# Kernel optimization log

Hardware: AMD Instinct MI355X
Metric: run time of the kernel (lower is better)

The kernel has to match this reference:

```python
import jax, jax.numpy as jnp
import numpy as np
import math

H, E, HD = 12, 768, 64   # heads, embed_dim, per-head hidden
B, S, L = 8, 512, 512    # batch, dec len, enc len
EPS = 1e-12


def layer_norm(x, w, b):
    u = jnp.mean(x, axis=-1, keepdims=True)
    s = jnp.mean((x - u) ** 2, axis=-1, keepdims=True)
    return w * (x - u) / jnp.sqrt(s + EPS) + b


def gelu(x):
    return x * 0.5 * (1.0 + jax.lax.erf(x / math.sqrt(2.0)))


def attention(k, q, w_k, w_q, pw, pb, mask):
    # k:[b,kl,E] q:[b,ql,E] w_k/w_q:[H,E,HD] mask broadcastable to [b,H,ql,kl]
    kx = jnp.einsum('ble,hed->bhld', k, w_k)
    qx = jnp.einsum('bqe,hed->bhqd', q, w_q)
    score = jnp.einsum('bhqd,bhkd->bhqk', qx, kx) / math.sqrt(HD)
    score = jnp.where(mask, score, jnp.asarray(-1e4, score.dtype))
    attn = jax.nn.softmax(score, axis=-1)
    out = jnp.einsum('bhqk,bhkd->bhqd', attn, kx)  # values are kx (as in source)
    b_, h, ql, d = out.shape
    out = out.transpose(0, 2, 1, 3).reshape(b_, ql, h * d)
    return out @ pw + pb


def setup_inputs() -> dict:
    key = jax.random.key(0)
    ks = jax.random.split(key, 16)
    xav = lambda k, shp, fan: jax.random.normal(k, shp, jnp.float32) * math.sqrt(2.0 / fan)
    inp = {
        'X': jax.random.normal(ks[0], (B, S, E), jnp.float32),
        'enc_outputs': jax.random.normal(ks[1], (B, L, E), jnp.float32),
        'enc_valid_lens': jax.random.randint(ks[2], (B,), 1, L + 1, jnp.int32),
        'w_kx1': xav(ks[3], (H, E, HD), E + HD),
        'w_qx1': xav(ks[4], (H, E, HD), E + HD),
        'proj1_w': xav(ks[5], (H * HD, E), 2 * E),
        'proj1_b': jnp.zeros((E,), jnp.float32),
        'ln1_w': jnp.ones((E,), jnp.float32),
        'ln1_b': jnp.zeros((E,), jnp.float32),
        'w_kx2': xav(ks[6], (H, E, HD), E + HD),
        'w_qx2': xav(ks[7], (H, E, HD), E + HD),
        'proj2_w': xav(ks[8], (H * HD, E), 2 * E),
        'proj2_b': jnp.zeros((E,), jnp.float32),
        'ln2_w': jnp.ones((E,), jnp.float32),
        'ln2_b': jnp.zeros((E,), jnp.float32),
        'ffn_w1': xav(ks[9], (E, E), 2 * E),
        'ffn_b1': jnp.zeros((E,), jnp.float32),
        'ffn_w2': xav(ks[10], (E, E), 2 * E),
        'ffn_b2': jnp.zeros((E,), jnp.float32),
        'ln3_w': jnp.ones((E,), jnp.float32),
        'ln3_b': jnp.zeros((E,), jnp.float32),
    }
    return inp


def reference(X, enc_outputs, enc_valid_lens,
              w_kx1, w_qx1, proj1_w, proj1_b, ln1_w, ln1_b,
              w_kx2, w_qx2, proj2_w, proj2_b, ln2_w, ln2_b,
              ffn_w1, ffn_b1, ffn_w2, ffn_b2, ln3_w, ln3_b):
    s = X.shape[1]
    # training path: dec_valid_lens is 2D -> causal mask in Attention
    causal = jnp.tril(jnp.ones((s, s), dtype=bool))[None, None]          # [1,1,s,s]
    X2 = attention(X, X, w_kx1, w_qx1, proj1_w, proj1_b, causal)
    Y = layer_norm(X2 + X, ln1_w, ln1_b)
    # cross mask: key padding from enc_valid_lens (1D branch)
    kl = enc_outputs.shape[1]
    pad = (jnp.arange(kl)[None] < enc_valid_lens[:, None])[:, None, None]  # [b,1,1,kl]
    Y2 = attention(enc_outputs, Y, w_kx2, w_qx2, proj2_w, proj2_b, pad)
    Z = layer_norm(Y2 + Y, ln2_w, ln2_b)
    F = gelu(Z @ ffn_w1 + ffn_b1) @ ffn_w2 + ffn_b2
    return layer_norm(F + Z, ln3_w, ln3_b)
```

## Files before the change

kernel.cpp:

```cpp
#include <hip/hip_runtime.h>
#include <hip/hip_bf16.h>

typedef __hip_bfloat16 bf16;
typedef __attribute__((ext_vector_type(8))) short s8v;
typedef __attribute__((ext_vector_type(4))) short s4v;
typedef __attribute__((ext_vector_type(4))) float f4v;

#define H_ 12
#define E_ 768
#define HD_ 64
#define B_ 8
#define S_ 512
#define M_ 4096

struct P9 { const void* s[8]; bf16* d[8]; const void* vs[10]; bf16* vd[10]; };

typedef __attribute__((address_space(3))) void lds_void;
typedef const __attribute__((address_space(1))) void g_void;

__device__ __forceinline__ void async_copy16(const bf16* g, short* l) {
    __builtin_amdgcn_global_load_lds((g_void*)g, (lds_void*)l, 16, 0, 0);
}

__device__ __forceinline__ float sh2f(short v) {
    unsigned int u = ((unsigned int)(unsigned short)v) << 16;
    return __uint_as_float(u);
}

__global__ void detect_kernel(const unsigned int* __restrict__ X, int* flag) {
    __shared__ int cnt;
    if (threadIdx.x == 0) cnt = 0;
    __syncthreads();
    int good = 0;
    for (int i = threadIdx.x; i < 16384; i += 256) {
        unsigned e = (X[i] >> 7) & 0xFFu;
        good += (e >= 100u && e <= 141u) ? 1 : 0;
    }
    atomicAdd(&cnt, good);
    __syncthreads();
    if (threadIdx.x == 0) *flag = (cnt > 9830) ? 0 : 1;
}

__global__ void conv2_kernel(const void* s0, const void* s1, bf16* d0, bf16* d1,
                             const int* __restrict__ flag) {
    const int fp32 = *flag;
    const void* s = blockIdx.y ? s1 : s0;
    bf16* d = blockIdx.y ? d1 : d0;
    int i = (blockIdx.x * 256 + threadIdx.x) * 4;
    if (fp32) {
        float4 v = *(const float4*)((const float*)s + i);
        bf16 a = __float2bfloat16(v.x), b = __float2bfloat16(v.y),
             c = __float2bfloat16(v.z), e = __float2bfloat16(v.w);
        s4v o = { *(short*)&a, *(short*)&b, *(short*)&c, *(short*)&e };
        *(s4v*)(d + i) = o;
    } else {
        *(s4v*)(d + i) = *(const s4v*)((const bf16*)s + i);
    }
}

__device__ __forceinline__ bf16 ldcvt(const void* s, int i, int fp32) {
    return fp32 ? __float2bfloat16(((const float*)s)[i]) : ((const bf16*)s)[i];
}

__global__ void repack_kernel(P9 p, const int* __restrict__ flag) {
    const int fp32 = *flag;
    const int z = blockIdx.z;
    if (z == 8) {
        int id = blockIdx.y * 12 + blockIdx.x;
        if (id < 10) {
            const void* s = p.vs[id];
            bf16* d = p.vd[id];
            for (int i = threadIdx.x; i < E_; i += 256) d[i] = ldcvt(s, i, fp32);
        }
        return;
    }
    __shared__ float t[64][65];
    const int c = threadIdx.x & 63, r0 = threadIdx.x >> 6;
    if (z < 4) {
        const void* s = p.s[z];
        bf16* d = p.d[z];
        const int e0 = blockIdx.x * 64, h = blockIdx.y;
        #pragma unroll
        for (int j = 0; j < 16; ++j) {
            int r = r0 * 16 + j;
            int idx = (h * E_ + e0 + r) * HD_ + c;
            t[r][c] = fp32 ? ((const float*)s)[idx] : __bfloat162float(((const bf16*)s)[idx]);
        }
        __syncthreads();
        #pragma unroll
        for (int j = 0; j < 16; ++j) {
            int r = r0 * 16 + j;
            d[(size_t)(h * 64 + r) * E_ + e0 + c] = __float2bfloat16(t[c][r]);
        }
    } else {
        const void* s = p.s[z];
        bf16* d = p.d[z];
        const int k0 = blockIdx.x * 64, n0 = blockIdx.y * 64;
        #pragma unroll
        for (int j = 0; j < 16; ++j) {
            int r = r0 * 16 + j;
            int idx = (k0 + r) * E_ + n0 + c;
            t[r][c] = fp32 ? ((const float*)s)[idx] : __bfloat162float(((const bf16*)s)[idx]);
        }
        __syncthreads();
        #pragma unroll
        for (int j = 0; j < 16; ++j) {
            int r = r0 * 16 + j;
            d[(size_t)(n0 + r) * E_ + k0 + c] = __float2bfloat16(t[c][r]);
        }
    }
}

__global__ void ktrans_kernel(const bf16* __restrict__ K1, const bf16* __restrict__ K2,
                              bf16* __restrict__ KT1, bf16* __restrict__ KT2) {
    __shared__ short t[64 * 72];
    const bf16* src = blockIdx.z ? K2 : K1;
    bf16* dst = blockIdx.z ? KT2 : KT1;
    const int s0 = blockIdx.x * 64, bh = blockIdx.y;
    const int b = bh / H_, h = bh % H_;
    const int tid = threadIdx.x;
    #pragma unroll
    for (int it = 0; it < 2; ++it) {
        int idx = tid * 2 + it;
        int row = idx >> 3, ch = (idx & 7) * 8;
        s8v v = *(const s8v*)(src + ((size_t)(b * S_ + s0 + row) * H_ + h) * HD_ + ch);
        *(s8v*)&t[row * 72 + ch] = v;
    }
    __syncthreads();
    const int orow = tid >> 2, oc = (tid & 3) * 16;
    s8v o0, o1;
    #pragma unroll
    for (int j = 0; j < 8; ++j) o0[j] = t[(oc + j) * 72 + orow];
    #pragma unroll
    for (int j = 0; j < 8; ++j) o1[j] = t[(oc + 8 + j) * 72 + orow];
    bf16* dp = dst + (size_t)(bh * 64 + orow) * S_ + s0 + oc;
    *(s8v*)dp = o0;
    *(s8v*)(dp + 8) = o1;
}

template <int EPI>
__global__ __launch_bounds__(256, 4) void gemm4(const bf16* __restrict__ A,
                                                const bf16* __restrict__ Aalt,
                                                const bf16* __restrict__ Bt,
                                                bf16* __restrict__ C,
                                                bf16* __restrict__ C2,
                                                bf16* __restrict__ C3,
                                                const bf16* __restrict__ bias,
                                                const bf16* __restrict__ res) {
    __shared__ short As[64 * 64];
    __shared__ short Bs[96 * 64];
    const int bm = blockIdx.x, bn = blockIdx.y;
    const int tid = threadIdx.x;
    const int w = tid >> 6, l = tid & 63;
    const int wr = (w >> 1) * 32, wc = (w & 1) * 48;
    const int lc = l & 15, quad = l >> 4;
    const int srA = l >> 3, slot = l & 7;
    const int kc = (slot ^ srA) * 8;

    const bf16* Ap = (EPI == 3 && bn >= 16) ? Aalt : A;

    f4v acc[2][3] = {};

    for (int k0 = 0; k0 < E_; k0 += 64) {
        #pragma unroll
        for (int c = 0; c < 5; ++c) {
            int seg = w * 5 + c;
            if (seg < 8) {
                int row = seg * 8 + srA;
                async_copy16(Ap + (size_t)(bm * 64 + row) * E_ + k0 + kc, &As[seg * 512]);
            } else {
                int row = (seg - 8) * 8 + srA;
                async_copy16(Bt + (size_t)(bn * 96 + row) * E_ + k0 + kc, &Bs[(seg - 8) * 512]);
            }
        }
        __syncthreads();

        #pragma unroll
        for (int kk = 0; kk < 2; ++kk) {
            s8v a[2], b[3];
            #pragma unroll
            for (int t = 0; t < 2; ++t) {
                int ar = wr + t * 16 + lc;
                a[t] = *(const s8v*)&As[ar * 64 + (((kk * 4 + quad) ^ (ar & 7)) * 8)];
            }
            #pragma unroll
            for (int t = 0; t < 3; ++t) {
                int bc = wc + t * 16 + lc;
                b[t] = *(const s8v*)&Bs[bc * 64 + (((kk * 4 + quad) ^ (bc & 7)) * 8)];
            }
            #pragma unroll
            for (int mt = 0; mt < 2; ++mt)
                #pragma unroll
                for (int nt = 0; nt < 3; ++nt)
                    acc[mt][nt] = __builtin_amdgcn_mfma_f32_16x16x32_bf16(a[mt], b[nt], acc[mt][nt], 0, 0, 0);
        }
        __syncthreads();
    }

    bf16* Co = C;
    int coff = 0;
    if (EPI == 3) {
        if (bn < 8)       { Co = C;  coff = 0; }
        else if (bn < 16) { Co = C2; coff = 768; }
        else              { Co = C3; coff = 1536; }
    }

    #pragma unroll
    for (int mt = 0; mt < 2; ++mt)
        #pragma unroll
        for (int nt = 0; nt < 3; ++nt)
            #pragma unroll
            for (int i = 0; i < 4; ++i) {
                int row = bm * 64 + wr + mt * 16 + quad * 4 + i;
                int col = bn * 96 + wc + nt * 16 + lc;
                float v = acc[mt][nt][i];
                if (EPI == 1)
                    v += __bfloat162float(bias[col]) + __bfloat162float(res[(size_t)row * E_ + col]);
                if (EPI == 2) {
                    v += __bfloat162float(bias[col]);
                    v = 0.5f * v * (1.0f + erff(v * 0.70710678118654752f));
                }
                if (EPI == 3) Co[(size_t)row * E_ + (col - coff)] = __float2bfloat16(v);
                else          C[(size_t)row * E_ + col] = __float2bfloat16(v);
            }
}

template <bool CAUSAL>
__global__ __launch_bounds__(256) void attn_kernel(const bf16* __restrict__ Q,
                                                   const bf16* __restrict__ Kx,
                                                   const bf16* __restrict__ KT,
                                                   bf16* __restrict__ O,
                                                   const int* __restrict__ vlen) {
    __shared__ short qs[64 * 64];
    __shared__ short ks[64 * 64];
    __shared__ short kts[64 * 64];
    __shared__ short ps[64 * 72];

    const int bh = blockIdx.x, qt = blockIdx.y;
    const int h = bh % H_, b = bh / H_;
    const int tid = threadIdx.x, w = tid >> 6, l = tid & 63;
    const int lr = (l >> 4) * 4, lc = l & 15, quad = l >> 4;
    const int srA = l >> 3, slot = l & 7;
    const int kc = (slot ^ srA) * 8;

    #pragma unroll
    for (int c = 0; c < 2; ++c) {
        int seg = w * 2 + c;
        int row = seg * 8 + srA;
        async_copy16(Q + ((size_t)(b * S_ + qt * 64 + row) * H_ + h) * HD_ + kc, &qs[seg * 512]);
    }

    const int valid = CAUSAL ? S_ : vlen[b];
    const int kmax = CAUSAL ? (qt + 1) : ((valid + 63) >> 6);

    float m_i[4], l_i[4];
    for (int i = 0; i < 4; i++) { m_i[i] = -3.0e38f; l_i[i] = 0.0f; }
    f4v o_acc[4] = {};

    for (int kt = 0; kt < kmax; ++kt) {
        #pragma unroll
        for (int c = 0; c < 2; ++c) {
            int seg = w * 2 + c;
            int row = seg * 8 + srA;
            async_copy16(Kx + ((size_t)(b * S_ + kt * 64 + row) * H_ + h) * HD_ + kc, &ks[seg * 512]);
            async_copy16(KT + (size_t)(bh * 64 + row) * S_ + kt * 64 + kc, &kts[seg * 512]);
        }
        __syncthreads();

        f4v sacc[4] = {};
        const int rq = w * 16 + lc;
        s8v aq0 = *(const s8v*)&qs[rq * 64 + ((quad ^ (rq & 7)) * 8)];
        s8v aq1 = *(const s8v*)&qs[rq * 64 + (((4 + quad) ^ (rq & 7)) * 8)];
        #pragma unroll
        for (int nt = 0; nt < 4; nt++) {
            int rk = nt * 16 + lc;
            s8v bk0 = *(const s8v*)&ks[rk * 64 + ((quad ^ (rk & 7)) * 8)];
            s8v bk1 = *(const s8v*)&ks[rk * 64 + (((4 + quad) ^ (rk & 7)) * 8)];
            sacc[nt] = __builtin_amdgcn_mfma_f32_16x16x32_bf16(aq0, bk0, sacc[nt], 0, 0, 0);
            sacc[nt] = __builtin_amdgcn_mfma_f32_16x16x32_bf16(aq1, bk1, sacc[nt], 0, 0, 0);
        }

        #pragma unroll
        for (int i = 0; i < 4; i++) {
            int qabs = qt * 64 + w * 16 + lr + i;
            float sv[4];
            float mx = -3.0e38f;
            #pragma unroll
            for (int nt = 0; nt < 4; nt++) {
                int kabs = kt * 64 + nt * 16 + lc;
                float s = sacc[nt][i] * 0.125f;
                bool ok = CAUSAL ? (kabs <= qabs) : (kabs < valid);
                sv[nt] = ok ? s : -1.0e4f;
                mx = fmaxf(mx, sv[nt]);
            }
            #pragma unroll
            for (int off = 1; off < 16; off <<= 1) mx = fmaxf(mx, __shfl_xor(mx, off));
            float mnew = fmaxf(m_i[i], mx);
            float alpha = __expf(m_i[i] - mnew);
            float psum = 0.0f;
            #pragma unroll
            for (int nt = 0; nt < 4; nt++) {
                float p = __expf(sv[nt] - mnew);
                psum += p;
                *(bf16*)&ps[(w * 16 + lr + i) * 72 + nt * 16 + lc] = __float2bfloat16(p);
            }
            #pragma unroll
            for (int off = 1; off < 16; off <<= 1) psum += __shfl_xor(psum, off);
            l_i[i] = l_i[i] * alpha + psum;
            m_i[i] = mnew;
            #pragma unroll
            for (int dt = 0; dt < 4; dt++) o_acc[dt][i] *= alpha;
        }

        s8v ap0 = *(const s8v*)&ps[rq * 72 + quad * 8];
        s8v ap1 = *(const s8v*)&ps[rq * 72 + 32 + quad * 8];
        #pragma unroll
        for (int dt = 0; dt < 4; dt++) {
            int rd = dt * 16 + lc;
            s8v bv0 = *(const s8v*)&kts[rd * 64 + ((quad ^ (rd & 7)) * 8)];
            s8v bv1 = *(const s8v*)&kts[rd * 64 + (((4 + quad) ^ (rd & 7)) * 8)];
            o_acc[dt] = __builtin_amdgcn_mfma_f32_16x16x32_bf16(ap0, bv0, o_acc[dt], 0, 0, 0);
            o_acc[dt] = __builtin_amdgcn_mfma_f32_16x16x32_bf16(ap1, bv1, o_acc[dt], 0, 0, 0);
        }
        __syncthreads();
    }

    #pragma unroll
    for (int dt = 0; dt < 4; dt++)
        #pragma unroll
        for (int i = 0; i < 4; i++) {
            int q = qt * 64 + w * 16 + lr + i;
            int d = dt * 16 + lc;
            float v = o_acc[dt][i] / l_i[i];
            O[((size_t)(b * S_ + q) * H_ + h) * HD_ + d] = __float2bfloat16(v);
        }
}

__global__ __launch_bounds__(256) void ln2_kernel(const bf16* __restrict__ X,
                                                  const bf16* __restrict__ wv,
                                                  const bf16* __restrict__ bv,
                                                  bf16* __restrict__ outb,
                                                  float* __restrict__ outf,
                                                  const int* __restrict__ flag) {
    const int row = blockIdx.x * 4 + (threadIdx.x >> 6);
    const int l = threadIdx.x & 63;
    const bf16* xr = X + (size_t)row * E_;
    s8v v8 = *(const s8v*)(xr + l * 8);
    s4v v4 = *(const s4v*)(xr + 512 + l * 4);
    float x[12];
    #pragma unroll
    for (int j = 0; j < 8; ++j) x[j] = sh2f(v8[j]);
    #pragma unroll
    for (int j = 0; j < 4; ++j) x[8 + j] = sh2f(v4[j]);
    float s = 0.f, ss = 0.f;
    #pragma unroll
    for (int j = 0; j < 12; ++j) { s += x[j]; ss += x[j] * x[j]; }
    #pragma unroll
    for (int off = 1; off < 64; off <<= 1) {
        s += __shfl_xor(s, off);
        ss += __shfl_xor(ss, off);
    }
    float mu = s * (1.0f / E_);
    float var = ss * (1.0f / E_) - mu * mu;
    float rstd = rsqrtf(fmaxf(var, 0.0f) + 1e-12f);
    const bool f32out = (outf != nullptr) && (*flag != 0);
    #pragma unroll
    for (int j = 0; j < 12; ++j) {
        int c = (j < 8) ? (l * 8 + j) : (512 + l * 4 + (j - 8));
        float v = (x[j] - mu) * rstd * __bfloat162float(wv[c]) + __bfloat162float(bv[c]);
        if (f32out) outf[(size_t)row * E_ + c] = v;
        else        outb[(size_t)row * E_ + c] = __float2bfloat16(v);
    }
}

extern "C" void kernel_launch(void* const* d_in, const int* in_sizes, int n_in,
                              void* d_out, int out_size, void* d_ws, size_t ws_size,
                              hipStream_t stream) {
    const void* X = d_in[0];
    const void* enc = d_in[1];
    const int* vlen = (const int*)d_in[2];

    char* ws = (char*)d_ws;
    int* flag = (int*)ws;
    bf16* vecs = (bf16*)(ws + 256);
    char* wbase = ws + 16384;
    const size_t WSZ = (size_t)E_ * E_ * sizeof(bf16);
    bf16* wk1 = (bf16*)(wbase + 0 * WSZ);
    bf16* wq1 = (bf16*)(wbase + 1 * WSZ);
    bf16* wk2 = (bf16*)(wbase + 2 * WSZ);
    bf16* wq2 = (bf16*)(wbase + 3 * WSZ);
    bf16* p1t = (bf16*)(wbase + 4 * WSZ);
    bf16* p2t = (bf16*)(wbase + 5 * WSZ);
    bf16* f1t = (bf16*)(wbase + 6 * WSZ);
    bf16* f2t = (bf16*)(wbase + 7 * WSZ);
    const size_t ASZ = (size_t)M_ * E_ * sizeof(bf16);
    char* abase = wbase + 8 * WSZ;
    bf16* Xc   = (bf16*)(abase + 0 * ASZ);
    bf16* ENCc = (bf16*)(abase + 1 * ASZ);
    bf16* A0  = (bf16*)(abase + 2 * ASZ);
    bf16* A1  = (bf16*)(abase + 3 * ASZ);
    bf16* A2  = (bf16*)(abase + 4 * ASZ);
    bf16* A3  = (bf16*)(abase + 5 * ASZ);
    bf16* A4  = (bf16*)(abase + 6 * ASZ);
    bf16* A5  = (bf16*)(abase + 7 * ASZ);
    bf16* KT1 = (bf16*)(abase + 8 * ASZ);
    bf16* KT2 = (bf16*)(abase + 9 * ASZ);

    bf16* bias1 = vecs + 0 * E_;
    bf16* lw1   = vecs + 1 * E_;
    bf16* lb1   = vecs + 2 * E_;
    bf16* bias2 = vecs + 3 * E_;
    bf16* lw2   = vecs + 4 * E_;
    bf16* lb2   = vecs + 5 * E_;
    bf16* fb1   = vecs + 6 * E_;
    bf16* fb2   = vecs + 7 * E_;
    bf16* lw3   = vecs + 8 * E_;
    bf16* lb3   = vecs + 9 * E_;

    detect_kernel<<<1, 256, 0, stream>>>((const unsigned int*)X, flag);
    conv2_kernel<<<dim3(M_ * E_ / 1024, 2), 256, 0, stream>>>(X, enc, Xc, ENCc, flag);

    P9 rp;
    rp.s[0] = d_in[3];  rp.d[0] = wk1;
    rp.s[1] = d_in[4];  rp.d[1] = wq1;
    rp.s[2] = d_in[9];  rp.d[2] = wk2;
    rp.s[3] = d_in[10]; rp.d[3] = wq2;
    rp.s[4] = d_in[5];  rp.d[4] = p1t;
    rp.s[5] = d_in[11]; rp.d[5] = p2t;
    rp.s[6] = d_in[15]; rp.d[6] = f1t;
    rp.s[7] = d_in[17]; rp.d[7] = f2t;
    rp.vs[0] = d_in[6];  rp.vd[0] = bias1;
    rp.vs[1] = d_in[7];  rp.vd[1] = lw1;
    rp.vs[2] = d_in[8];  rp.vd[2] = lb1;
    rp.vs[3] = d_in[12]; rp.vd[3] = bias2;
    rp.vs[4] = d_in[13]; rp.vd[4] = lw2;
    rp.vs[5] = d_in[14]; rp.vd[5] = lb2;
    rp.vs[6] = d_in[16]; rp.vd[6] = fb1;
    rp.vs[7] = d_in[18]; rp.vd[7] = fb2;
    rp.vs[8] = d_in[19]; rp.vd[8] = lw3;
    rp.vs[9] = d_in[20]; rp.vd[9] = lb3;
    repack_kernel<<<dim3(12, 12, 9), 256, 0, stream>>>(rp, flag);

    gemm4<3><<<dim3(64, 24), 256, 0, stream>>>(Xc, ENCc, wk1, A0, A1, A4, nullptr, nullptr);
    ktrans_kernel<<<dim3(8, 96, 2), 256, 0, stream>>>(A0, A4, KT1, KT2);

    attn_kernel<true><<<dim3(96, 8), 256, 0, stream>>>(A1, A0, KT1, A2, nullptr);
    gemm4<1><<<dim3(64, 8), 256, 0, stream>>>(A2, nullptr, p1t, A3, nullptr, nullptr, bias1, Xc);
    ln2_kernel<<<M_ / 4, 256, 0, stream>>>(A3, lw1, lb1, A5, nullptr, flag);

    gemm4<0><<<dim3(64, 8), 256, 0, stream>>>(A5, nullptr, wq2, A1, nullptr, nullptr, nullptr, nullptr);
    attn_kernel<false><<<dim3(96, 8), 256, 0, stream>>>(A1, A4, KT2, A2, vlen);
    gemm4<1><<<dim3(64, 8), 256, 0, stream>>>(A2, nullptr, p2t, A3, nullptr, nullptr, bias2, A5);
    ln2_kernel<<<M_ / 4, 256, 0, stream>>>(A3, lw2, lb2, A0, nullptr, flag);

    gemm4<2><<<dim3(64, 8), 256, 0, stream>>>(A0, nullptr, f1t, A1, nullptr, nullptr, fb1, nullptr);
    gemm4<1><<<dim3(64, 8), 256, 0, stream>>>(A1, nullptr, f2t, A2, nullptr, nullptr, fb2, A0);
    ln2_kernel<<<M_ / 4, 256, 0, stream>>>(A2, lw3, lb3, (bf16*)d_out, (float*)d_out, flag);
}
```

Baseline: 316.5 us.

## Fuse K transpose into projection GEMM and shrink GEMM tiles to 64x64

Replaces the separate K-transpose kernel by writing transposed K tiles from the QK projection GEMM epilogue through shared memory. All GEMMs switch from 64x96 to 64x64 tiles, giving more blocks per launch (12 column blocks instead of 8) at the cost of less reuse per block. The attention kernel also hoists the Q fragment loads out of the key loop. This removes one launch plus a full K read/write pass, while adding an extra LDS round trip and a sync in the projection epilogue.

```diff
diff --git a/kernel.cpp b/kernel.cpp
--- a/kernel.cpp
+++ b/kernel.cpp
@@ -25,6 +25,11 @@
 __device__ __forceinline__ float sh2f(short v) {
     unsigned int u = ((unsigned int)(unsigned short)v) << 16;
     return __uint_as_float(u);
+}
+
+__device__ __forceinline__ short f2sh(float v) {
+    bf16 b = __float2bfloat16(v);
+    return *(short*)&b;
 }
 
 __global__ void detect_kernel(const unsigned int* __restrict__ X, int* flag) {
@@ -111,108 +116,60 @@
     }
 }
 
-__global__ void ktrans_kernel(const bf16* __restrict__ K1, const bf16* __restrict__ K2,
-                              bf16* __restrict__ KT1, bf16* __restrict__ KT2) {
-    __shared__ short t[64 * 72];
-    const bf16* src = blockIdx.z ? K2 : K1;
-    bf16* dst = blockIdx.z ? KT2 : KT1;
-    const int s0 = blockIdx.x * 64, bh = blockIdx.y;
-    const int b = bh / H_, h = bh % H_;
-    const int tid = threadIdx.x;
-    #pragma unroll
-    for (int it = 0; it < 2; ++it) {
-        int idx = tid * 2 + it;
-        int row = idx >> 3, ch = (idx & 7) * 8;
-        s8v v = *(const s8v*)(src + ((size_t)(b * S_ + s0 + row) * H_ + h) * HD_ + ch);
-        *(s8v*)&t[row * 72 + ch] = v;
-    }
-    __syncthreads();
-    const int orow = tid >> 2, oc = (tid & 3) * 16;
-    s8v o0, o1;
-    #pragma unroll
-    for (int j = 0; j < 8; ++j) o0[j] = t[(oc + j) * 72 + orow];
-    #pragma unroll
-    for (int j = 0; j < 8; ++j) o1[j] = t[(oc + 8 + j) * 72 + orow];
-    bf16* dp = dst + (size_t)(bh * 64 + orow) * S_ + s0 + oc;
-    *(s8v*)dp = o0;
-    *(s8v*)(dp + 8) = o1;
-}
-
 template <int EPI>
-__global__ __launch_bounds__(256, 4) void gemm4(const bf16* __restrict__ A,
-                                                const bf16* __restrict__ Aalt,
+__global__ __launch_bounds__(256, 4) void gemm3(const bf16* __restrict__ A,
                                                 const bf16* __restrict__ Bt,
                                                 bf16* __restrict__ C,
-                                                bf16* __restrict__ C2,
-                                                bf16* __restrict__ C3,
                                                 const bf16* __restrict__ bias,
                                                 const bf16* __restrict__ res) {
     __shared__ short As[64 * 64];
-    __shared__ short Bs[96 * 64];
+    __shared__ short Bs[64 * 64];
     const int bm = blockIdx.x, bn = blockIdx.y;
     const int tid = threadIdx.x;
     const int w = tid >> 6, l = tid & 63;
-    const int wr = (w >> 1) * 32, wc = (w & 1) * 48;
+    const int wr = (w >> 1) * 32, wc = (w & 1) * 32;
     const int lc = l & 15, quad = l >> 4;
     const int srA = l >> 3, slot = l & 7;
     const int kc = (slot ^ srA) * 8;
 
-    const bf16* Ap = (EPI == 3 && bn >= 16) ? Aalt : A;
-
-    f4v acc[2][3] = {};
+    f4v acc[2][2] = {};
 
     for (int k0 = 0; k0 < E_; k0 += 64) {
         #pragma unroll
-        for (int c = 0; c < 5; ++c) {
-            int seg = w * 5 + c;
-            if (seg < 8) {
-                int row = seg * 8 + srA;
-                async_copy16(Ap + (size_t)(bm * 64 + row) * E_ + k0 + kc, &As[seg * 512]);
-            } else {
-                int row = (seg - 8) * 8 + srA;
-                async_copy16(Bt + (size_t)(bn * 96 + row) * E_ + k0 + kc, &Bs[(seg - 8) * 512]);
-            }
+        for (int c = 0; c < 2; ++c) {
+            int seg = w * 2 + c;
+            int row = seg * 8 + srA;
+            async_copy16(A + (size_t)(bm * 64 + row) * E_ + k0 + kc, &As[seg * 512]);
+            async_copy16(Bt + (size_t)(bn * 64 + row) * E_ + k0 + kc, &Bs[seg * 512]);
         }
         __syncthreads();
 
         #pragma unroll
         for (int kk = 0; kk < 2; ++kk) {
-            s8v a[2], b[3];
+            s8v a[2], b[2];
             #pragma unroll
             for (int t = 0; t < 2; ++t) {
                 int ar = wr + t * 16 + lc;
                 a[t] = *(const s8v*)&As[ar * 64 + (((kk * 4 + quad) ^ (ar & 7)) * 8)];
-            }
-            #pragma unroll
-            for (int t = 0; t < 3; ++t) {
                 int bc = wc + t * 16 + lc;
                 b[t] = *(const s8v*)&Bs[bc * 64 + (((kk * 4 + quad) ^ (bc & 7)) * 8)];
             }
-            #pragma unroll
-            for (int mt = 0; mt < 2; ++mt)
-                #pragma unroll
-                for (int nt = 0; nt < 3; ++nt)
-                    acc[mt][nt] = __builtin_amdgcn_mfma_f32_16x16x32_bf16(a[mt], b[nt], acc[mt][nt], 0, 0, 0);
-        }
-        __syncthreads();
-    }
-
-    bf16* Co = C;
-    int coff = 0;
-    if (EPI == 3) {
-        if (bn < 8)       { Co = C;  coff = 0; }
-        else if (bn < 16) { Co = C2; coff = 768; }
-        else              { Co = C3; coff = 1536; }
+            acc[0][0] = __builtin_amdgcn_mfma_f32_16x16x32_bf16(a[0], b[0], acc[0][0], 0, 0, 0);
+            acc[0][1] = __builtin_amdgcn_mfma_f32_16x16x32_bf16(a[0], b[1], acc[0][1], 0, 0, 0);
+            acc[1][0] = __builtin_amdgcn_mfma_f32_16x16x32_bf16(a[1], b[0], acc[1][0], 0, 0, 0);
+            acc[1][1] = __builtin_amdgcn_mfma_f32_16x16x32_bf16(a[1], b[1], acc[1][1], 0, 0, 0);
+        }
+        __syncthreads();
     }
 
     #pragma unroll
     for (int mt = 0; mt < 2; ++mt)
         #pragma unroll
-        for (int nt = 0; nt < 3; ++nt)
+        for (int nt = 0; nt < 2; ++nt)
             #pragma unroll
             for (int i = 0; i < 4; ++i) {
                 int row = bm * 64 + wr + mt * 16 + quad * 4 + i;
-                int col = bn * 96 + wc + nt * 16 + lc;
+                int col = bn * 64 + wc + nt * 16 + lc;
                 float v = acc[mt][nt][i];
                 if (EPI == 1)
                     v += __bfloat162float(bias[col]) + __bfloat162float(res[(size_t)row * E_ + col]);
@@ -220,9 +177,97 @@
                     v += __bfloat162float(bias[col]);
                     v = 0.5f * v * (1.0f + erff(v * 0.70710678118654752f));
                 }
-                if (EPI == 3) Co[(size_t)row * E_ + (col - coff)] = __float2bfloat16(v);
-                else          C[(size_t)row * E_ + col] = __float2bfloat16(v);
+                C[(size_t)row * E_ + col] = __float2bfloat16(v);
             }
+}
+
+__global__ __launch_bounds__(256, 4) void gemm3q(const bf16* __restrict__ Xc,
+                                                 const bf16* __restrict__ ENCc,
+                                                 const bf16* __restrict__ Bt,
+                                                 bf16* __restrict__ K1,
+                                                 bf16* __restrict__ Q1,
+                                                 bf16* __restrict__ K2,
+                                                 bf16* __restrict__ KT1,
+                                                 bf16* __restrict__ KT2) {
+    __shared__ short sm[8192];
+    short* As = sm;
+    short* Bs = sm + 4096;
+    const int bm = blockIdx.x, bn = blockIdx.y;
+    const int tid = threadIdx.x;
+    const int w = tid >> 6, l = tid & 63;
+    const int wr = (w >> 1) * 32, wc = (w & 1) * 32;
+    const int lc = l & 15, quad = l >> 4;
+    const int srA = l >> 3, slot = l & 7;
+    const int kc = (slot ^ srA) * 8;
+
+    const bf16* A = (bn >= 24) ? ENCc : Xc;
+
+    f4v acc[2][2] = {};
+
+    for (int k0 = 0; k0 < E_; k0 += 64) {
+        #pragma unroll
+        for (int c = 0; c < 2; ++c) {
+            int seg = w * 2 + c;
+            int row = seg * 8 + srA;
+            async_copy16(A + (size_t)(bm * 64 + row) * E_ + k0 + kc, &As[seg * 512]);
+            async_copy16(Bt + (size_t)(bn * 64 + row) * E_ + k0 + kc, &Bs[seg * 512]);
+        }
+        __syncthreads();
+
+        #pragma unroll
+        for (int kk = 0; kk < 2; ++kk) {
+            s8v a[2], b[2];
+            #pragma unroll
+            for (int t = 0; t < 2; ++t) {
+                int ar = wr + t * 16 + lc;
+                a[t] = *(const s8v*)&As[ar * 64 + (((kk * 4 + quad) ^ (ar & 7)) * 8)];
+                int bc = wc + t * 16 + lc;
+                b[t] = *(const s8v*)&Bs[bc * 64 + (((kk * 4 + quad) ^ (bc & 7)) * 8)];
+            }
+            acc[0][0] = __builtin_amdgcn_mfma_f32_16x16x32_bf16(a[0], b[0], acc[0][0], 0, 0, 0);
+            acc[0][1] = __builtin_amdgcn_mfma_f32_16x16x32_bf16(a[0], b[1], acc[0][1], 0, 0, 0);
+            acc[1][0] = __builtin_amdgcn_mfma_f32_16x16x32_bf16(a[1], b[0], acc[1][0], 0, 0, 0);
+            acc[1][1] = __builtin_amdgcn_mfma_f32_16x16x32_bf16(a[1], b[1], acc[1][1], 0, 0, 0);
+        }
+        __syncthreads();
+    }
+
+    const int band = (bn < 12) ? 0 : (bn < 24) ? 1 : 2;
+    const int nb = bn - band * 12;
+    bf16* C = (band == 0) ? K1 : (band == 1) ? Q1 : K2;
+
+    #pragma unroll
+    for (int mt = 0; mt < 2; ++mt)
+        #pragma unroll
+        for (int nt = 0; nt < 2; ++nt)
+            #pragma unroll
+            for (int i = 0; i < 4; ++i) {
+                int row = bm * 64 + wr + mt * 16 + quad * 4 + i;
+                int col = nb * 64 + wc + nt * 16 + lc;
+                C[(size_t)row * E_ + col] = __float2bfloat16(acc[mt][nt][i]);
+            }
+
+    if (band != 1) {
+        bf16* KT = (band == 0) ? KT1 : KT2;
+        #pragma unroll
+        for (int mt = 0; mt < 2; ++mt)
+            #pragma unroll
+            for (int nt = 0; nt < 2; ++nt)
+                #pragma unroll
+                for (int i = 0; i < 4; ++i) {
+                    int srow = wr + mt * 16 + quad * 4 + i;
+                    int d = wc + nt * 16 + lc;
+                    sm[d * 72 + srow] = f2sh(acc[mt][nt][i]);
+                }
+        __syncthreads();
+        const int drow = tid >> 2, c0 = (tid & 3) * 16;
+        s8v o0 = *(const s8v*)&sm[drow * 72 + c0];
+        s8v o1 = *(const s8v*)&sm[drow * 72 + c0 + 8];
+        const int b = bm >> 3, s0 = (bm & 7) * 64;
+        bf16* dp = KT + ((size_t)((b * H_ + nb) * 64 + drow) * S_) + s0 + c0;
+        *(s8v*)dp = o0;
+        *(s8v*)(dp + 8) = o1;
+    }
 }
 
 template <bool CAUSAL>
@@ -242,6 +287,7 @@
     const int lr = (l >> 4) * 4, lc = l & 15, quad = l >> 4;
     const int srA = l >> 3, slot = l & 7;
     const int kc = (slot ^ srA) * 8;
+    const int rq = w * 16 + lc;
 
     #pragma unroll
     for (int c = 0; c < 2; ++c) {
@@ -256,6 +302,7 @@
     float m_i[4], l_i[4];
     for (int i = 0; i < 4; i++) { m_i[i] = -3.0e38f; l_i[i] = 0.0f; }
     f4v o_acc[4] = {};
+    s8v aq0, aq1;
 
     for (int kt = 0; kt < kmax; ++kt) {
         #pragma unroll
@@ -267,10 +314,12 @@
         }
         __syncthreads();
 
+        if (kt == 0) {
+            aq0 = *(const s8v*)&qs[rq * 64 + ((quad ^ (rq & 7)) * 8)];
+            aq1 = *(const s8v*)&qs[rq * 64 + (((4 + quad) ^ (rq & 7)) * 8)];
+        }
+
         f4v sacc[4] = {};
-        const int rq = w * 16 + lc;
-        s8v aq0 = *(const s8v*)&qs[rq * 64 + ((quad ^ (rq & 7)) * 8)];
-        s8v aq1 = *(const s8v*)&qs[rq * 64 + (((4 + quad) ^ (rq & 7)) * 8)];
         #pragma unroll
         for (int nt = 0; nt < 4; nt++) {
             int rk = nt * 16 + lc;
@@ -302,7 +351,7 @@
             for (int nt = 0; nt < 4; nt++) {
                 float p = __expf(sv[nt] - mnew);
                 psum += p;
-                *(bf16*)&ps[(w * 16 + lr + i) * 72 + nt * 16 + lc] = __float2bfloat16(p);
+                ps[(w * 16 + lr + i) * 72 + nt * 16 + lc] = f2sh(p);
             }
             #pragma unroll
             for (int off = 1; off < 16; off <<= 1) psum += __shfl_xor(psum, off);
@@ -441,19 +490,18 @@
     rp.vs[9] = d_in[20]; rp.vd[9] = lb3;
     repack_kernel<<<dim3(12, 12, 9), 256, 0, stream>>>(rp, flag);
 
-    gemm4<3><<<dim3(64, 24), 256, 0, stream>>>(Xc, ENCc, wk1, A0, A1, A4, nullptr, nullptr);
-    ktrans_kernel<<<dim3(8, 96, 2), 256, 0, stream>>>(A0, A4, KT1, KT2);
+    gemm3q<<<dim3(64, 36), 256, 0, stream>>>(Xc, ENCc, wk1, A0, A1, A4, KT1, KT2);
 
     attn_kernel<true><<<dim3(96, 8), 256, 0, stream>>>(A1, A0, KT1, A2, nullptr);
-    gemm4<1><<<dim3(64, 8), 256, 0, stream>>>(A2, nullptr, p1t, A3, nullptr, nullptr, bias1, Xc);
+    gemm3<1><<<dim3(64, 12), 256, 0, stream>>>(A2, p1t, A3, bias1, Xc);
     ln2_kernel<<<M_ / 4, 256, 0, stream>>>(A3, lw1, lb1, A5, nullptr, flag);
 
-    gemm4<0><<<dim3(64, 8), 256, 0, stream>>>(A5, nullptr, wq2, A1, nullptr, nullptr, nullptr, nullptr);
+    gemm3<0><<<dim3(64, 12), 256, 0, stream>>>(A5, wq2, A1, nullptr, nullptr);
     attn_kernel<false><<<dim3(96, 8), 256, 0, stream>>>(A1, A4, KT2, A2, vlen);
-    gemm4<1><<<dim3(64, 8), 256, 0, stream>>>(A2, nullptr, p2t, A3, nullptr, nullptr, bias2, A5);
+    gemm3<1><<<dim3(64, 12), 256, 0, stream>>>(A2, p2t, A3, bias2, A5);
     ln2_kernel<<<M_ / 4, 256, 0, stream>>>(A3, lw2, lb2, A0, nullptr, flag);
 
-    gemm4<2><<<dim3(64, 8), 256, 0, stream>>>(A0, nullptr, f1t, A1, nullptr, nullptr, fb1, nullptr);
-    gemm4<1><<<dim3(64, 8), 256, 0, stream>>>(A1, nullptr, f2t, A2, nullptr, nullptr, fb2, A0);
+    gemm3<2><<<dim3(64, 12), 256, 0, stream>>>(A0, f1t, A1, fb1, nullptr);
+    gemm3<1><<<dim3(64, 12), 256, 0, stream>>>(A1, f2t, A2, fb2, A0);
     ln2_kernel<<<M_ / 4, 256, 0, stream>>>(A2, lw3, lb3, (bf16*)d_out, (float*)d_out, flag);
 }
```

Result: faster. 294.1 us (-7.1%).
